# Optimization experiments

Measured on AMD Instinct MI355X. Metric: run time of the kernel, lower is better.

## Reference

```python
import jax, jax.numpy as jnp
import numpy as np

B, S, D = 2, 2048, 4096
H, HD = 32, 128  # n_heads, head_dim
P = 30           # prefix_len
ROPE_THETA = 10000.0


def _rope_tables():
    inv = 1.0 / (ROPE_THETA ** (np.arange(0, HD, 2, dtype=np.float64) / HD))
    f = np.outer(np.arange(S, dtype=np.float64), inv)  # [S, HD/2]
    return jnp.asarray(np.cos(f), jnp.float32), jnp.asarray(np.sin(f), jnp.float32)


def setup_inputs() -> dict:
    key = jax.random.key(0)
    ks = jax.random.split(key, 7)
    scale = 0.02
    x = jax.random.normal(ks[0], (B, S, D), jnp.float32)
    freqs_cos, freqs_sin = _rope_tables()
    prefix = jax.random.normal(ks[1], (1, P, D), jnp.float32) * scale
    prefix_gate = jax.random.normal(ks[2], (H,), jnp.float32) * 0.1
    wq = jax.random.normal(ks[3], (D, H * HD), jnp.float32) * scale
    wk = jax.random.normal(ks[4], (D, H * HD), jnp.float32) * scale
    wv = jax.random.normal(ks[5], (D, H * HD), jnp.float32) * scale
    wo = jax.random.normal(ks[6], (H * HD, D), jnp.float32) * scale
    return dict(x=x, freqs_cos=freqs_cos, freqs_sin=freqs_sin, prefix=prefix,
                prefix_gate=prefix_gate, wq=wq, wk=wk, wv=wv, wo=wo, start_pos=0)


def _apply_rope(t, cos, sin):
    # t: [b, s, h, hd]; cos/sin: [s, hd/2] -> broadcast [1, s, 1, hd/2]
    tr = t.reshape(*t.shape[:-1], HD // 2, 2)
    t0, t1 = tr[..., 0], tr[..., 1]
    c = cos[None, :, None, :]
    s = sin[None, :, None, :]
    o0 = t0 * c - t1 * s
    o1 = t0 * s + t1 * c
    return jnp.stack([o0, o1], axis=-1).reshape(t.shape)


def _attend(q, k, v, causal):
    # q: [b, sq, h, d]; k, v: [b, sk, h, d]
    scale = 1.0 / jnp.sqrt(jnp.asarray(HD, q.dtype))
    scores = jnp.einsum('bqhd,bkhd->bhqk', q, k) * scale
    if causal:
        sq, sk = q.shape[1], k.shape[1]
        mask = jnp.tril(jnp.ones((sq, sk), bool))
        scores = jnp.where(mask[None, None], scores, jnp.asarray(-1e30, scores.dtype))
    probs = jax.nn.softmax(scores, axis=-1)
    return jnp.einsum('bhqk,bkhd->bqhd', probs, v)


def reference(x, freqs_cos, freqs_sin, prefix, prefix_gate, wq, wk, wv, wo, start_pos):
    bsz, seqlen, _ = x.shape
    xq = (x @ wq).reshape(bsz, seqlen, H, HD)
    xk = (x @ wk).reshape(bsz, seqlen, H, HD)
    xv = (x @ wv).reshape(bsz, seqlen, H, HD)
    xq = _apply_rope(xq, freqs_cos, freqs_sin)
    xk = _apply_rope(xk, freqs_cos, freqs_sin)
    # n_rep == 1 (MHA), repeat_kv is identity
    out = _attend(xq, xk, xv, causal=True)  # [b, s, h, hd]
    # prefix-tuning branch: no RoPE on prefix k/v, non-causal attention
    pk = jnp.broadcast_to(prefix @ wk, (bsz, P, H * HD)).reshape(bsz, P, H, HD)
    pv = jnp.broadcast_to(prefix @ wv, (bsz, P, H * HD)).reshape(bsz, P, H, HD)
    prefix_delta = _attend(xq, pk, pv, causal=False)
    gate = jnp.tanh(prefix_gate).reshape(1, 1, H, 1)
    out = out + gate * prefix_delta
    out = out.reshape(bsz, seqlen, H * HD)
    return out @ wo
```

## Files before the change

kernel.cpp:

```cpp
#include <hip/hip_runtime.h>
#include <hip/hip_bf16.h>

#define AS1 __attribute__((address_space(1)))
#define AS3 __attribute__((address_space(3)))

typedef __attribute__((ext_vector_type(8))) short bf16x8;
typedef __attribute__((ext_vector_type(4))) float f32x4;

#define B_ 2
#define S_ 2048
#define D_ 4096
#define H_ 32
#define HD_ 128
#define P_ 30

__device__ __forceinline__ short f2b(float f) {
  union { __hip_bfloat16 h; short s; } u;
  u.h = __float2bfloat16(f);
  return u.s;
}
__device__ __forceinline__ float b2f(short s) {
  union { short s; __hip_bfloat16 h; } u;
  u.s = s;
  return __bfloat162float(u.h);
}
__device__ __forceinline__ void gload16(const void* g, void* l) {
  __builtin_amdgcn_global_load_lds((const AS1 void*)g, (AS3 void*)l, 16, 0, 0);
}

__global__ __launch_bounds__(256) void convert_f32_bf16(const float* __restrict__ in,
                                                        short* __restrict__ out) {
  size_t i = ((size_t)blockIdx.x * 256 + threadIdx.x) * 4;
  float4 v = *reinterpret_cast<const float4*>(in + i);
  short4 o;
  o.x = f2b(v.x); o.y = f2b(v.y); o.z = f2b(v.z); o.w = f2b(v.w);
  *reinterpret_cast<short4*>(out + i) = o;
}

__global__ __launch_bounds__(256) void pad_prefix(const float* __restrict__ p,
                                                  short* __restrict__ pb) {
  int i = blockIdx.x * 256 + threadIdx.x;
  int row = i >> 12, col = i & 4095;
  pb[i] = (row < P_) ? f2b(p[row * D_ + col]) : (short)0;
}

__global__ void transpose_convert(const float* __restrict__ W, short* __restrict__ Wt,
                                  int K, int N) {
  __shared__ float t[32][33];
  int bx = blockIdx.x, by = blockIdx.y;
  int tx = threadIdx.x, ty = threadIdx.y;
#pragma unroll
  for (int i = 0; i < 4; ++i) {
    int r = ty * 4 + i;
    t[r][tx] = W[(size_t)(by * 32 + r) * N + bx * 32 + tx];
  }
  __syncthreads();
#pragma unroll
  for (int i = 0; i < 4; ++i) {
    int r = ty * 4 + i;
    Wt[(size_t)(bx * 32 + r) * K + by * 32 + tx] = f2b(t[tx][r]);
  }
}

__global__ __launch_bounds__(256) void rope_kernel(short* __restrict__ t,
                                                   const float* __restrict__ fc,
                                                   const float* __restrict__ fs) {
  size_t g = ((size_t)blockIdx.x * 256 + threadIdx.x) * 8;
  int d = (int)(g & 127);
  int s = (int)((g >> 12) & 2047);
  bf16x8 v = *reinterpret_cast<bf16x8*>(t + g);
  int i0 = d >> 1;
  float4 c = *reinterpret_cast<const float4*>(fc + (size_t)s * 64 + i0);
  float4 sn = *reinterpret_cast<const float4*>(fs + (size_t)s * 64 + i0);
  float cc[4] = {c.x, c.y, c.z, c.w};
  float ss[4] = {sn.x, sn.y, sn.z, sn.w};
  bf16x8 o;
#pragma unroll
  for (int p = 0; p < 4; ++p) {
    float t0 = b2f(v[2 * p]), t1 = b2f(v[2 * p + 1]);
    o[2 * p] = f2b(t0 * cc[p] - t1 * ss[p]);
    o[2 * p + 1] = f2b(t0 * ss[p] + t1 * cc[p]);
  }
  *reinterpret_cast<bf16x8*>(t + g) = o;
}

template <int OM>
__global__ __launch_bounds__(256) void gemm_bt(const short* __restrict__ A,
                                               const short* __restrict__ Bt,
                                               void* __restrict__ Cv,
                                               int M, int N, int K) {
  __shared__ short As[128 * 32];
  __shared__ short Bs[128 * 32];
  const int tid = threadIdx.x;
  const int lane = tid & 63;
  const int wbase = tid & 192;
  const int wr = ((tid >> 7) & 1) * 64;
  const int wc = ((tid >> 6) & 1) * 64;
  const int lr = lane & 15;
  const int lk = (lane >> 4) * 8;
  int lin = blockIdx.y * gridDim.x + blockIdx.x;
  int nwg = gridDim.x * gridDim.y;
  int cpx = nwg >> 3;
  int swz = (lin & 7) * cpx + (lin >> 3);
  const int bm = swz / gridDim.x, bn = swz % gridDim.x;
  f32x4 acc[4][4] = {};
  const short* Ab = A + (size_t)bm * 128 * K;
  const short* Bb = Bt + (size_t)bn * 128 * K;
  for (int kt = 0; kt < K; kt += 32) {
    __syncthreads();
#pragma unroll
    for (int i = 0; i < 2; ++i) {
      int f = i * 256 + tid;
      int row = f >> 2, col = (f & 3) * 8;
      gload16(Ab + (size_t)row * K + kt + col, &As[(i * 256 + wbase) * 8]);
      gload16(Bb + (size_t)row * K + kt + col, &Bs[(i * 256 + wbase) * 8]);
    }
    __syncthreads();
    bf16x8 af[4], bfr[4];
#pragma unroll
    for (int m = 0; m < 4; ++m)
      af[m] = *reinterpret_cast<const bf16x8*>(&As[(wr + m * 16 + lr) * 32 + lk]);
#pragma unroll
    for (int n = 0; n < 4; ++n)
      bfr[n] = *reinterpret_cast<const bf16x8*>(&Bs[(wc + n * 16 + lr) * 32 + lk]);
#pragma unroll
    for (int m = 0; m < 4; ++m)
#pragma unroll
      for (int n = 0; n < 4; ++n)
        acc[m][n] = __builtin_amdgcn_mfma_f32_16x16x32_bf16(af[m], bfr[n], acc[m][n], 0, 0, 0);
  }
  const int row0 = bm * 128 + wr + (lane >> 4) * 4;
  const int col0 = bn * 128 + wc + lr;
#pragma unroll
  for (int m = 0; m < 4; ++m)
#pragma unroll
    for (int n = 0; n < 4; ++n)
#pragma unroll
      for (int j = 0; j < 4; ++j) {
        size_t idx = (size_t)(row0 + m * 16 + j) * N + col0 + n * 16;
        if constexpr (OM == 1) ((short*)Cv)[idx] = f2b(acc[m][n][j]);
        else ((float*)Cv)[idx] = acc[m][n][j];
      }
}

#define PHASE(mh, kh, STAGE, TAIL)                                              \
  {                                                                             \
    bf16x8 af[4], bfr[4];                                                       \
    const int pg = (((kh)*4 + lg) ^ (lr & 7)) * 8;                              \
    _Pragma("unroll") for (int mm = 0; mm < 4; ++mm)                            \
      af[mm] = *(const bf16x8*)&As[slot][(wr + (mh)*64 + mm*16 + lr)*64 + pg];  \
    _Pragma("unroll") for (int nn = 0; nn < 4; ++nn)                            \
      bfr[nn] = *(const bf16x8*)&Bs[slot][(wc + nn*16 + lr)*64 + pg];           \
    STAGE;                                                                      \
    __builtin_amdgcn_s_barrier();                                               \
    asm volatile("s_waitcnt lgkmcnt(0)" ::: "memory");                          \
    __builtin_amdgcn_sched_barrier(0);                                          \
    __builtin_amdgcn_s_setprio(1);                                              \
    _Pragma("unroll") for (int mm = 0; mm < 4; ++mm)                            \
      _Pragma("unroll") for (int nn = 0; nn < 4; ++nn)                          \
        acc[(mh)*4 + mm][nn] = __builtin_amdgcn_mfma_f32_16x16x32_bf16(         \
            af[mm], bfr[nn], acc[(mh)*4 + mm][nn], 0, 0, 0);                    \
    __builtin_amdgcn_s_setprio(0);                                              \
    TAIL;                                                                       \
    __builtin_amdgcn_s_barrier();                                               \
  }

template <int OM>
__global__ __launch_bounds__(512, 2) void gemm256(const short* __restrict__ A,
                                                  const short* __restrict__ Bt,
                                                  void* __restrict__ Cv,
                                                  int M, int N, int K) {
  __shared__ short As[2][256 * 64];
  __shared__ short Bs[2][256 * 64];
  const int tid = threadIdx.x;
  const int w = tid >> 6;
  const int lane = tid & 63;
  const int lr = lane & 15, lg = lane >> 4;
  const int wr = (w >> 2) * 128;
  const int wc = (w & 3) * 64;
  int lin = blockIdx.y * gridDim.x + blockIdx.x;
  int nwg = gridDim.x * gridDim.y;
  int cpx = nwg >> 3;
  int swz = (lin & 7) * cpx + (lin >> 3);
  const int bm = swz / gridDim.x, bn = swz % gridDim.x;

  const short* Ab = A + (size_t)bm * 256 * K;
  const short* Bb = Bt + (size_t)bn * 256 * K;
  const int NT = K >> 6;

  f32x4 acc[8][4] = {};

  auto stA = [&](int slot_, int r0, int kt) {
    int row = r0 + (lane >> 3);
    int gsrc = (lane & 7) ^ ((lane >> 3) & 7);
    gload16(Ab + (size_t)row * K + kt + gsrc * 8, &As[slot_][r0 * 64]);
  };
  auto stB = [&](int slot_, int r0, int kt) {
    int row = r0 + (lane >> 3);
    int gsrc = (lane & 7) ^ ((lane >> 3) & 7);
    gload16(Bb + (size_t)row * K + kt + gsrc * 8, &Bs[slot_][r0 * 64]);
  };

  const int q2 = w * 2, q4 = w * 4;
  const int rt0 = (q2 < 8 ? 0 : 64) + q2 * 8;
  const int rt1 = (q2 + 1 < 8 ? 0 : 64) + (q2 + 1) * 8;

  {
#pragma unroll
    for (int i = 0; i < 4; ++i) stB(0, (q4 + i) * 8, 0);
    stA(0, rt0, 0); stA(0, 64 + rt0, 0);
    stA(0, rt1, 0); stA(0, 64 + rt1, 0);
#pragma unroll
    for (int i = 0; i < 4; ++i) stB(1, (q4 + i) * 8, 64);
    stA(1, rt0, 64); stA(1, 64 + rt0, 64);
    stA(1, rt1, 64); stA(1, 64 + rt1, 64);
  }
  asm volatile("s_waitcnt vmcnt(8)" ::: "memory");
  __builtin_amdgcn_s_barrier();

  for (int t = 0; t < NT; ++t) {
    const int slot = t & 1;
    const int ns = slot ^ 1;
    const int kt1 = (t + 1) << 6, kt2 = (t + 2) << 6;
    const bool s6 = (t >= 1) && (t + 1 < NT);
    const bool s2 = (t + 2 < NT);

    PHASE(0, 0,
          { if (s6) { stB(ns, (q4 + 0) * 8, kt1); stB(ns, (q4 + 1) * 8, kt1); } },
          {});
    PHASE(0, 1,
          { if (s6) { stB(ns, (q4 + 2) * 8, kt1); stB(ns, (q4 + 3) * 8, kt1);
                      stA(ns, 64 + rt0, kt1);     stA(ns, 64 + rt1, kt1); } },
          {});
    PHASE(1, 0,
          { if (s2) stA(slot, rt0, kt2); },
          {});
    PHASE(1, 1,
          { if (s2) stA(slot, rt1, kt2); },
          { if (s2) asm volatile("s_waitcnt vmcnt(2)" ::: "memory");
            else    asm volatile("s_waitcnt vmcnt(0)" ::: "memory"); });
  }

  const int row0 = bm * 256 + wr + lg * 4;
  const int col0 = bn * 256 + wc + lr;
  if constexpr (OM == 2) {
    short* C = (short*)Cv;
#pragma unroll
    for (int mf = 0; mf < 8; ++mf)
#pragma unroll
      for (int n = 0; n < 4; ++n) {
        int r0 = row0 + mf * 16;
        int bb = r0 >> 11, s0 = r0 & 2047;
        short4 pk;
        pk.x = f2b(acc[mf][n][0]); pk.y = f2b(acc[mf][n][1]);
        pk.z = f2b(acc[mf][n][2]); pk.w = f2b(acc[mf][n][3]);
        size_t idx = ((size_t)(bb * 4096 + col0 + n * 16)) * 2048 + s0;
        *reinterpret_cast<short4*>(&C[idx]) = pk;
      }
  } else {
#pragma unroll
    for (int mf = 0; mf < 8; ++mf)
#pragma unroll
      for (int n = 0; n < 4; ++n)
#pragma unroll
        for (int j = 0; j < 4; ++j) {
          size_t idx = (size_t)(row0 + mf * 16 + j) * N + col0 + n * 16;
          if constexpr (OM == 1) ((short*)Cv)[idx] = f2b(acc[mf][n][j]);
          else ((float*)Cv)[idx] = acc[mf][n][j];
        }
  }
}

__global__ __launch_bounds__(1024, 4) void attn_kernel(
    const short* __restrict__ qb, const short* __restrict__ kb, const short* __restrict__ vt,
    short* __restrict__ ab) {
  __shared__ short Ks[2][64 * 128];
  __shared__ short Vs[128 * 64];
  __shared__ short Ps[16][16 * 64];
  const int tid = threadIdx.x;
  const int wave = tid >> 6, lane = tid & 63;
  const int lr = lane & 15, lg = lane >> 4;
  const int lin = blockIdx.x;
  const int qt = 7 - (lin >> 6);
  const int bh = lin & 63;
  const int b = bh >> 5, h = bh & 31;

  bf16x8 aq[4];
  {
    const short* qrow = qb + ((size_t)(b * S_ + qt * 256 + wave * 16 + lr) * H_ + h) * HD_;
#pragma unroll
    for (int kk = 0; kk < 4; ++kk)
      aq[kk] = *reinterpret_cast<const bf16x8*>(qrow + kk * 32 + lg * 8);
  }

  float m = -1e30f, l = 0.f;
  f32x4 o[8] = {};

  const short* kb_bh = kb + ((size_t)b * S_ * H_ + h) * HD_;
  const short* vt_bh = vt + ((size_t)(b * H_ + h)) * HD_ * S_;

  auto stageK = [&](int t, int buf) {
    int row = tid >> 4;
    int col = ((tid & 15) ^ (row & 7)) * 8;
    gload16(kb_bh + (size_t)(t * 64 + row) * (H_ * HD_) + col,
            &Ks[buf][(tid & 960) * 8]);
  };
  auto loadV = [&](int t, bf16x8& vr) {
    int row = tid >> 3;
    vr = *reinterpret_cast<const bf16x8*>(vt_bh + (size_t)row * S_ + t * 64 + (tid & 7) * 8);
  };
  auto writeV = [&](const bf16x8& vr) {
    int row = tid >> 3;
    int gran = (tid & 7) ^ (row & 7);
    *reinterpret_cast<bf16x8*>(&Vs[row * 64 + gran * 8]) = vr;
  };

  auto process = [&](int t, bool diag) {
    const int buf = t & 1;
    f32x4 sc[4] = {};
    __builtin_amdgcn_s_setprio(1);
#pragma unroll
    for (int cb = 0; cb < 4; ++cb) {
      int tok = cb * 16 + lr;
#pragma unroll
      for (int kk = 0; kk < 4; ++kk) {
        int addr = tok * 128 + (((kk * 4 + lg) ^ (tok & 7)) * 8);
        bf16x8 bk = *reinterpret_cast<const bf16x8*>(&Ks[buf][addr]);
        sc[cb] = __builtin_amdgcn_mfma_f32_16x16x32_bf16(bk, aq[kk], sc[cb], 0, 0, 0);
      }
    }
    __builtin_amdgcn_s_setprio(0);
    const float scale = 0.08838834764831845f;
    const int rowg = qt * 256 + wave * 16 + lr;
#pragma unroll
    for (int cb = 0; cb < 4; ++cb)
#pragma unroll
      for (int j = 0; j < 4; ++j) {
        int colg = t * 64 + cb * 16 + lg * 4 + j;
        float v = sc[cb][j] * scale;
        sc[cb][j] = (!diag || colg <= rowg) ? v : -1e30f;
      }
    float mx = sc[0][0];
#pragma unroll
    for (int cb = 0; cb < 4; ++cb)
#pragma unroll
      for (int j = 0; j < 4; ++j) mx = fmaxf(mx, sc[cb][j]);
    mx = fmaxf(mx, __shfl_xor(mx, 16));
    mx = fmaxf(mx, __shfl_xor(mx, 32));
    float mn = fmaxf(m, mx);
    float alpha = __expf(m - mn);
    m = mn;
    float rs = 0.f;
#pragma unroll
    for (int cb = 0; cb < 4; ++cb) {
      short4 pk;
      float p0 = __expf(sc[cb][0] - mn);
      float p1 = __expf(sc[cb][1] - mn);
      float p2 = __expf(sc[cb][2] - mn);
      float p3 = __expf(sc[cb][3] - mn);
      rs += (p0 + p1) + (p2 + p3);
      pk.x = f2b(p0); pk.y = f2b(p1); pk.z = f2b(p2); pk.w = f2b(p3);
      int gran = (cb * 2 + (lg >> 1)) ^ (lr & 7);
      *reinterpret_cast<short4*>(&Ps[wave][lr * 64 + gran * 8 + (lg & 1) * 4]) = pk;
    }
    rs += __shfl_xor(rs, 16);
    rs += __shfl_xor(rs, 32);
    l = l * alpha + rs;
    f32x4 av;
#pragma unroll
    for (int j = 0; j < 4; ++j) av[j] = __shfl(alpha, lg * 4 + j);
#pragma unroll
    for (int nb = 0; nb < 8; ++nb)
#pragma unroll
      for (int j = 0; j < 4; ++j) o[nb][j] *= av[j];
#pragma unroll
    for (int kk = 0; kk < 2; ++kk) {
      bf16x8 ap = *reinterpret_cast<const bf16x8*>(
          &Ps[wave][lr * 64 + (((kk * 4 + lg) ^ (lr & 7)) * 8)]);
      __builtin_amdgcn_s_setprio(1);
#pragma unroll
      for (int nb = 0; nb < 8; ++nb) {
        int d = nb * 16 + lr;
        bf16x8 bv = *reinterpret_cast<const bf16x8*>(
            &Vs[d * 64 + (((kk * 4 + lg) ^ (lr & 7)) * 8)]);
        o[nb] = __builtin_amdgcn_mfma_f32_16x16x32_bf16(ap, bv, o[nb], 0, 0, 0);
      }
      __builtin_amdgcn_s_setprio(0);
    }
  };

  const int nt = 4 * (qt + 1);
  bf16x8 vr;
  stageK(0, 0);
  loadV(0, vr);
  __syncthreads();
  writeV(vr);
  __syncthreads();
  for (int t = 0; t < nt; ++t) {
    const bool more = (t + 1 < nt);
    if (more) {
      loadV(t + 1, vr);
      stageK(t + 1, (t + 1) & 1);
    }
    process(t, t >= 4 * qt);
    __syncthreads();
    if (more) writeV(vr);
    __syncthreads();
  }

  {
    f32x4 lv;
#pragma unroll
    for (int j = 0; j < 4; ++j) lv[j] = __shfl(l, lg * 4 + j);
#pragma unroll
    for (int j = 0; j < 4; ++j) {
      int q = qt * 256 + wave * 16 + lg * 4 + j;
      float inv = 1.f / lv[j];
      size_t base = ((size_t)(b * S_ + q) * H_ + h) * HD_;
#pragma unroll
      for (int nb = 0; nb < 8; ++nb)
        ab[base + nb * 16 + lr] = f2b(o[nb][j] * inv);
    }
  }
}

__global__ __launch_bounds__(256) void prefix_kernel(
    const short* __restrict__ qb, const short* __restrict__ pkb, const short* __restrict__ pvb,
    const float* __restrict__ gate, short* __restrict__ ab) {
  __shared__ short pkl[P_ * 128];
  __shared__ short pvl[P_ * 128];
  const int tid = threadIdx.x;
  const int qt = blockIdx.x, bh = blockIdx.y;
  const int b = bh >> 5, h = bh & 31;
  for (int i = tid; i < P_ * 16; i += 256) {
    int row = i >> 4, c = (i & 15) * 8;
    *(bf16x8*)&pkl[row * 128 + c] = *(const bf16x8*)&pkb[(size_t)row * 4096 + h * 128 + c];
    *(bf16x8*)&pvl[row * 128 + c] = *(const bf16x8*)&pvb[(size_t)row * 4096 + h * 128 + c];
  }
  __syncthreads();
  const int r = tid >> 2, p = tid & 3;
  const int q = qt * 64 + r;
  const short* qrow = qb + ((size_t)(b * S_ + q) * H_ + h) * HD_ + p * 32;
  float qv[32];
#pragma unroll
  for (int i = 0; i < 4; ++i) {
    bf16x8 v = *(const bf16x8*)(qrow + i * 8);
#pragma unroll
    for (int e = 0; e < 8; ++e) qv[i * 8 + e] = b2f(v[e]);
  }
  const float scale = 0.08838834764831845f;
  float s[P_];
  float mx = -1e30f;
#pragma unroll
  for (int j = 0; j < P_; ++j) {
    float dot = 0.f;
#pragma unroll
    for (int i = 0; i < 4; ++i) {
      bf16x8 kv = *(const bf16x8*)&pkl[j * 128 + p * 32 + i * 8];
#pragma unroll
      for (int e = 0; e < 8; ++e) dot += qv[i * 8 + e] * b2f(kv[e]);
    }
    dot += __shfl_xor(dot, 1);
    dot += __shfl_xor(dot, 2);
    s[j] = dot * scale;
    mx = fmaxf(mx, s[j]);
  }
  float sum = 0.f;
#pragma unroll
  for (int j = 0; j < P_; ++j) { s[j] = __expf(s[j] - mx); sum += s[j]; }
  float o[32] = {};
#pragma unroll
  for (int j = 0; j < P_; ++j) {
#pragma unroll
    for (int i = 0; i < 4; ++i) {
      bf16x8 vv = *(const bf16x8*)&pvl[j * 128 + p * 32 + i * 8];
#pragma unroll
      for (int e = 0; e < 8; ++e) o[i * 8 + e] += s[j] * b2f(vv[e]);
    }
  }
  float g = tanhf(gate[h]) / sum;
  short* arow = ab + ((size_t)(b * S_ + q) * H_ + h) * HD_ + p * 32;
#pragma unroll
  for (int i = 0; i < 4; ++i) {
    bf16x8 av = *(bf16x8*)(arow + i * 8);
#pragma unroll
    for (int e = 0; e < 8; ++e) av[e] = f2b(b2f(av[e]) + g * o[i * 8 + e]);
    *(bf16x8*)(arow + i * 8) = av;
  }
}

extern "C" void kernel_launch(void* const* d_in, const int* in_sizes, int n_in,
                              void* d_out, int out_size, void* d_ws, size_t ws_size,
                              hipStream_t stream) {
  const float* x = (const float*)d_in[0];
  const float* fc = (const float*)d_in[1];
  const float* fs = (const float*)d_in[2];
  const float* prefix = (const float*)d_in[3];
  const float* gate = (const float*)d_in[4];
  const float* wq = (const float*)d_in[5];
  const float* wk = (const float*)d_in[6];
  const float* wv = (const float*)d_in[7];
  const float* wo = (const float*)d_in[8];
  float* out = (float*)d_out;

  char* ws = (char*)d_ws;
  const size_t SZ = (size_t)4096 * 4096 * 2;
  short* xb = (short*)(ws);
  short* wT = (short*)(ws + SZ);
  short* qbuf = (short*)(ws + 2 * SZ);
  short* kbuf = (short*)(ws + 3 * SZ);
  short* vT = (short*)(ws + 4 * SZ);
  short* pb = (short*)(ws + 5 * SZ);
  short* pkb = (short*)(ws + 5 * SZ + (1 << 20));
  short* pvb = (short*)(ws + 5 * SZ + (2 << 20));
  short* abuf = xb;

  dim3 tcg(128, 128), tcb(32, 8);
  dim3 gg(16, 16), gp(32, 1);

  convert_f32_bf16<<<16384, 256, 0, stream>>>(x, xb);
  pad_prefix<<<2048, 256, 0, stream>>>(prefix, pb);

  transpose_convert<<<tcg, tcb, 0, stream>>>(wq, wT, 4096, 4096);
  gemm256<1><<<gg, 512, 0, stream>>>(xb, wT, qbuf, 4096, 4096, 4096);

  transpose_convert<<<tcg, tcb, 0, stream>>>(wk, wT, 4096, 4096);
  gemm256<1><<<gg, 512, 0, stream>>>(xb, wT, kbuf, 4096, 4096, 4096);
  gemm_bt<1><<<gp, 256, 0, stream>>>(pb, wT, pkb, 128, 4096, 4096);

  transpose_convert<<<tcg, tcb, 0, stream>>>(wv, wT, 4096, 4096);
  gemm256<2><<<gg, 512, 0, stream>>>(xb, wT, vT, 4096, 4096, 4096);
  gemm_bt<1><<<gp, 256, 0, stream>>>(pb, wT, pvb, 128, 4096, 4096);

  rope_kernel<<<8192, 256, 0, stream>>>(qbuf, fc, fs);
  rope_kernel<<<8192, 256, 0, stream>>>(kbuf, fc, fs);

  attn_kernel<<<512, 1024, 0, stream>>>(qbuf, kbuf, vT, abuf);
  prefix_kernel<<<dim3(32, 64), 256, 0, stream>>>(qbuf, pkb, pvb, gate, abuf);

  transpose_convert<<<tcg, tcb, 0, stream>>>(wo, wT, 4096, 4096);
  gemm256<0><<<gg, 512, 0, stream>>>(abuf, wT, out, 4096, 4096, 4096);
}
```

Baseline: 1.020 ms.

## Fuse prefix attention into main attention kernel using MFMA with transposed prefix V

Removes the separate scalar prefix_kernel and computes the prefix branch inside attn_kernel as one extra 64-wide MFMA tile, with keys masked beyond the prefix length. Its normalized, gated result is added to the causal output before the single store. The prefix V GEMM gains a transposed bf16 output mode so it can be staged into the kernel's V layout. This avoids re-reading Q and doing a read-modify-write of the attention output, in exchange for extra registers (o2) in the attention kernel and padded-row compute. The gemm_bt epilogue's else-branch now always writes bf16, which only matters if float output was used there.

```diff
diff --git a/kernel.cpp b/kernel.cpp
--- a/kernel.cpp
+++ b/kernel.cpp
@@ -131,16 +131,29 @@
   }
   const int row0 = bm * 128 + wr + (lane >> 4) * 4;
   const int col0 = bn * 128 + wc + lr;
-#pragma unroll
-  for (int m = 0; m < 4; ++m)
-#pragma unroll
-    for (int n = 0; n < 4; ++n)
-#pragma unroll
-      for (int j = 0; j < 4; ++j) {
-        size_t idx = (size_t)(row0 + m * 16 + j) * N + col0 + n * 16;
-        if constexpr (OM == 1) ((short*)Cv)[idx] = f2b(acc[m][n][j]);
-        else ((float*)Cv)[idx] = acc[m][n][j];
+  if constexpr (OM == 3) {
+    short* C = (short*)Cv;
+#pragma unroll
+    for (int m = 0; m < 4; ++m)
+#pragma unroll
+      for (int n = 0; n < 4; ++n) {
+        short4 pk;
+        pk.x = f2b(acc[m][n][0]); pk.y = f2b(acc[m][n][1]);
+        pk.z = f2b(acc[m][n][2]); pk.w = f2b(acc[m][n][3]);
+        size_t idx = (size_t)(col0 + n * 16) * M + row0 + m * 16;
+        *reinterpret_cast<short4*>(&C[idx]) = pk;
       }
+  } else {
+#pragma unroll
+    for (int m = 0; m < 4; ++m)
+#pragma unroll
+      for (int n = 0; n < 4; ++n)
+#pragma unroll
+        for (int j = 0; j < 4; ++j) {
+          size_t idx = (size_t)(row0 + m * 16 + j) * N + col0 + n * 16;
+          ((short*)Cv)[idx] = f2b(acc[m][n][j]);
+        }
+  }
 }
 
 #define PHASE(mh, kh, STAGE, TAIL)                                              \
@@ -273,7 +286,8 @@
 
 __global__ __launch_bounds__(1024, 4) void attn_kernel(
     const short* __restrict__ qb, const short* __restrict__ kb, const short* __restrict__ vt,
-    short* __restrict__ ab) {
+    const short* __restrict__ pkb, const short* __restrict__ pvt,
+    const float* __restrict__ gate, short* __restrict__ ab) {
   __shared__ short Ks[2][64 * 128];
   __shared__ short Vs[128 * 64];
   __shared__ short Ps[16][16 * 64];
@@ -293,8 +307,8 @@
       aq[kk] = *reinterpret_cast<const bf16x8*>(qrow + kk * 32 + lg * 8);
   }
 
-  float m = -1e30f, l = 0.f;
-  f32x4 o[8] = {};
+  float m = -1e30f, l = 0.f, l2 = 0.f;
+  f32x4 o[8] = {}, o2[8] = {};
 
   const short* kb_bh = kb + ((size_t)b * S_ * H_ + h) * HD_;
   const short* vt_bh = vt + ((size_t)(b * H_ + h)) * HD_ * S_;
@@ -305,9 +319,18 @@
     gload16(kb_bh + (size_t)(t * 64 + row) * (H_ * HD_) + col,
             &Ks[buf][(tid & 960) * 8]);
   };
+  auto stagePK = [&](int buf) {
+    int row = tid >> 4;
+    int col = ((tid & 15) ^ (row & 7)) * 8;
+    gload16(pkb + (size_t)row * 4096 + h * HD_ + col, &Ks[buf][(tid & 960) * 8]);
+  };
   auto loadV = [&](int t, bf16x8& vr) {
     int row = tid >> 3;
     vr = *reinterpret_cast<const bf16x8*>(vt_bh + (size_t)row * S_ + t * 64 + (tid & 7) * 8);
+  };
+  auto loadPV = [&](bf16x8& vr) {
+    int row = tid >> 3;
+    vr = *reinterpret_cast<const bf16x8*>(pvt + ((size_t)h * HD_ + row) * 128 + (tid & 7) * 8);
   };
   auto writeV = [&](const bf16x8& vr) {
     int row = tid >> 3;
@@ -315,9 +338,9 @@
     *reinterpret_cast<bf16x8*>(&Vs[row * 64 + gran * 8]) = vr;
   };
 
-  auto process = [&](int t, bool diag) {
-    const int buf = t & 1;
-    f32x4 sc[4] = {};
+  const float scale = 0.08838834764831845f;
+
+  auto qkt = [&](int buf, f32x4 sc[4]) {
     __builtin_amdgcn_s_setprio(1);
 #pragma unroll
     for (int cb = 0; cb < 4; ++cb) {
@@ -330,7 +353,28 @@
       }
     }
     __builtin_amdgcn_s_setprio(0);
-    const float scale = 0.08838834764831845f;
+  };
+  auto pv = [&](f32x4* acc_) {
+#pragma unroll
+    for (int kk = 0; kk < 2; ++kk) {
+      bf16x8 ap = *reinterpret_cast<const bf16x8*>(
+          &Ps[wave][lr * 64 + (((kk * 4 + lg) ^ (lr & 7)) * 8)]);
+      __builtin_amdgcn_s_setprio(1);
+#pragma unroll
+      for (int nb = 0; nb < 8; ++nb) {
+        int d = nb * 16 + lr;
+        bf16x8 bv = *reinterpret_cast<const bf16x8*>(
+            &Vs[d * 64 + (((kk * 4 + lg) ^ (lr & 7)) * 8)]);
+        acc_[nb] = __builtin_amdgcn_mfma_f32_16x16x32_bf16(ap, bv, acc_[nb], 0, 0, 0);
+      }
+      __builtin_amdgcn_s_setprio(0);
+    }
+  };
+
+  auto process = [&](int t, bool diag) {
+    const int buf = t & 1;
+    f32x4 sc[4] = {};
+    qkt(buf, sc);
     const int rowg = qt * 256 + wave * 16 + lr;
 #pragma unroll
     for (int cb = 0; cb < 4; ++cb)
@@ -373,24 +417,57 @@
     for (int nb = 0; nb < 8; ++nb)
 #pragma unroll
       for (int j = 0; j < 4; ++j) o[nb][j] *= av[j];
-#pragma unroll
-    for (int kk = 0; kk < 2; ++kk) {
-      bf16x8 ap = *reinterpret_cast<const bf16x8*>(
-          &Ps[wave][lr * 64 + (((kk * 4 + lg) ^ (lr & 7)) * 8)]);
-      __builtin_amdgcn_s_setprio(1);
-#pragma unroll
-      for (int nb = 0; nb < 8; ++nb) {
-        int d = nb * 16 + lr;
-        bf16x8 bv = *reinterpret_cast<const bf16x8*>(
-            &Vs[d * 64 + (((kk * 4 + lg) ^ (lr & 7)) * 8)]);
-        o[nb] = __builtin_amdgcn_mfma_f32_16x16x32_bf16(ap, bv, o[nb], 0, 0, 0);
+    pv(o);
+  };
+
+  auto processPrefix = [&]() {
+    f32x4 sc[4] = {};
+    qkt(0, sc);
+#pragma unroll
+    for (int cb = 0; cb < 4; ++cb)
+#pragma unroll
+      for (int j = 0; j < 4; ++j) {
+        int coll = cb * 16 + lg * 4 + j;
+        float v = sc[cb][j] * scale;
+        sc[cb][j] = (coll < P_) ? v : -1e30f;
       }
-      __builtin_amdgcn_s_setprio(0);
-    }
+    float mx = sc[0][0];
+#pragma unroll
+    for (int cb = 0; cb < 4; ++cb)
+#pragma unroll
+      for (int j = 0; j < 4; ++j) mx = fmaxf(mx, sc[cb][j]);
+    mx = fmaxf(mx, __shfl_xor(mx, 16));
+    mx = fmaxf(mx, __shfl_xor(mx, 32));
+    float rs = 0.f;
+#pragma unroll
+    for (int cb = 0; cb < 4; ++cb) {
+      short4 pk;
+      float p0 = __expf(sc[cb][0] - mx);
+      float p1 = __expf(sc[cb][1] - mx);
+      float p2 = __expf(sc[cb][2] - mx);
+      float p3 = __expf(sc[cb][3] - mx);
+      rs += (p0 + p1) + (p2 + p3);
+      pk.x = f2b(p0); pk.y = f2b(p1); pk.z = f2b(p2); pk.w = f2b(p3);
+      int gran = (cb * 2 + (lg >> 1)) ^ (lr & 7);
+      *reinterpret_cast<short4*>(&Ps[wave][lr * 64 + gran * 8 + (lg & 1) * 4]) = pk;
+    }
+    rs += __shfl_xor(rs, 16);
+    rs += __shfl_xor(rs, 32);
+    l2 = rs;
+    pv(o2);
   };
 
   const int nt = 4 * (qt + 1);
   bf16x8 vr;
+
+  stagePK(0);
+  loadPV(vr);
+  __syncthreads();
+  writeV(vr);
+  __syncthreads();
+  processPrefix();
+  __syncthreads();
+
   stageK(0, 0);
   loadV(0, vr);
   __syncthreads();
@@ -409,83 +486,23 @@
   }
 
   {
-    f32x4 lv;
-#pragma unroll
-    for (int j = 0; j < 4; ++j) lv[j] = __shfl(l, lg * 4 + j);
+    float g = tanhf(gate[h]);
+    f32x4 lv, lv2;
+#pragma unroll
+    for (int j = 0; j < 4; ++j) {
+      lv[j] = __shfl(l, lg * 4 + j);
+      lv2[j] = __shfl(l2, lg * 4 + j);
+    }
 #pragma unroll
     for (int j = 0; j < 4; ++j) {
       int q = qt * 256 + wave * 16 + lg * 4 + j;
       float inv = 1.f / lv[j];
+      float inv2 = g / lv2[j];
       size_t base = ((size_t)(b * S_ + q) * H_ + h) * HD_;
 #pragma unroll
       for (int nb = 0; nb < 8; ++nb)
-        ab[base + nb * 16 + lr] = f2b(o[nb][j] * inv);
-    }
-  }
-}
-
-__global__ __launch_bounds__(256) void prefix_kernel(
-    const short* __restrict__ qb, const short* __restrict__ pkb, const short* __restrict__ pvb,
-    const float* __restrict__ gate, short* __restrict__ ab) {
-  __shared__ short pkl[P_ * 128];
-  __shared__ short pvl[P_ * 128];
-  const int tid = threadIdx.x;
-  const int qt = blockIdx.x, bh = blockIdx.y;
-  const int b = bh >> 5, h = bh & 31;
-  for (int i = tid; i < P_ * 16; i += 256) {
-    int row = i >> 4, c = (i & 15) * 8;
-    *(bf16x8*)&pkl[row * 128 + c] = *(const bf16x8*)&pkb[(size_t)row * 4096 + h * 128 + c];
-    *(bf16x8*)&pvl[row * 128 + c] = *(const bf16x8*)&pvb[(size_t)row * 4096 + h * 128 + c];
-  }
-  __syncthreads();
-  const int r = tid >> 2, p = tid & 3;
-  const int q = qt * 64 + r;
-  const short* qrow = qb + ((size_t)(b * S_ + q) * H_ + h) * HD_ + p * 32;
-  float qv[32];
-#pragma unroll
-  for (int i = 0; i < 4; ++i) {
-    bf16x8 v = *(const bf16x8*)(qrow + i * 8);
-#pragma unroll
-    for (int e = 0; e < 8; ++e) qv[i * 8 + e] = b2f(v[e]);
-  }
-  const float scale = 0.08838834764831845f;
-  float s[P_];
-  float mx = -1e30f;
-#pragma unroll
-  for (int j = 0; j < P_; ++j) {
-    float dot = 0.f;
-#pragma unroll
-    for (int i = 0; i < 4; ++i) {
-      bf16x8 kv = *(const bf16x8*)&pkl[j * 128 + p * 32 + i * 8];
-#pragma unroll
-      for (int e = 0; e < 8; ++e) dot += qv[i * 8 + e] * b2f(kv[e]);
-    }
-    dot += __shfl_xor(dot, 1);
-    dot += __shfl_xor(dot, 2);
-    s[j] = dot * scale;
-    mx = fmaxf(mx, s[j]);
-  }
-  float sum = 0.f;
-#pragma unroll
-  for (int j = 0; j < P_; ++j) { s[j] = __expf(s[j] - mx); sum += s[j]; }
-  float o[32] = {};
-#pragma unroll
-  for (int j = 0; j < P_; ++j) {
-#pragma unroll
-    for (int i = 0; i < 4; ++i) {
-      bf16x8 vv = *(const bf16x8*)&pvl[j * 128 + p * 32 + i * 8];
-#pragma unroll
-      for (int e = 0; e < 8; ++e) o[i * 8 + e] += s[j] * b2f(vv[e]);
-    }
-  }
-  float g = tanhf(gate[h]) / sum;
-  short* arow = ab + ((size_t)(b * S_ + q) * H_ + h) * HD_ + p * 32;
-#pragma unroll
-  for (int i = 0; i < 4; ++i) {
-    bf16x8 av = *(bf16x8*)(arow + i * 8);
-#pragma unroll
-    for (int e = 0; e < 8; ++e) av[e] = f2b(b2f(av[e]) + g * o[i * 8 + e]);
-    *(bf16x8*)(arow + i * 8) = av;
+        ab[base + nb * 16 + lr] = f2b(o[nb][j] * inv + o2[nb][j] * inv2);
+    }
   }
 }
 
@@ -512,7 +529,7 @@
   short* vT = (short*)(ws + 4 * SZ);
   short* pb = (short*)(ws + 5 * SZ);
   short* pkb = (short*)(ws + 5 * SZ + (1 << 20));
-  short* pvb = (short*)(ws + 5 * SZ + (2 << 20));
+  short* pvt = (short*)(ws + 5 * SZ + (2 << 20));
   short* abuf = xb;
 
   dim3 tcg(128, 128), tcb(32, 8);
@@ -530,13 +547,12 @@
 
   transpose_convert<<<tcg, tcb, 0, stream>>>(wv, wT, 4096, 4096);
   gemm256<2><<<gg, 512, 0, stream>>>(xb, wT, vT, 4096, 4096, 4096);
-  gemm_bt<1><<<gp, 256, 0, stream>>>(pb, wT, pvb, 128, 4096, 4096);
+  gemm_bt<3><<<gp, 256, 0, stream>>>(pb, wT, pvt, 128, 4096, 4096);
 
   rope_kernel<<<8192, 256, 0, stream>>>(qbuf, fc, fs);
   rope_kernel<<<8192, 256, 0, stream>>>(kbuf, fc, fs);
 
-  attn_kernel<<<512, 1024, 0, stream>>>(qbuf, kbuf, vT, abuf);
-  prefix_kernel<<<dim3(32, 64), 256, 0, stream>>>(qbuf, pkb, pvb, gate, abuf);
+  attn_kernel<<<512, 1024, 0, stream>>>(qbuf, kbuf, vT, pkb, pvt, gate, abuf);
 
   transpose_convert<<<tcg, tcb, 0, stream>>>(wo, wT, 4096, 4096);
   gemm256<0><<<gg, 512, 0, stream>>>(abuf, wT, out, 4096, 4096, 4096);
```

New measurement: 915.9 us. 1.11x faster.
